# Kernel tuning notes

Measured on AMD Instinct MI355X. Metric: run time of the kernel, lower is better.

## Reference

```python
import jax, jax.numpy as jnp
import numpy as np

NG = 8       # GroupNorm groups
EPS = 1e-5   # torch default eps for GroupNorm/BatchNorm
M_AND = 5    # Anderson history size
MAX_ITER = 25
LAM = 1e-4
BETA = 1.0


def conv2d(x, w):
    # x: [B,C,H,W], w: [O,I,3,3], stride 1, SAME padding (pad=1)
    return jax.lax.conv_general_dilated(x, w, (1, 1), 'SAME',
                                        dimension_numbers=('NCHW', 'OIHW', 'NCHW'))


def group_norm(x, g, b):
    B, C, H, W = x.shape
    xg = x.reshape(B, NG, C // NG, H, W)
    mu = xg.mean((2, 3, 4), keepdims=True)
    var = xg.var((2, 3, 4), keepdims=True)
    xn = ((xg - mu) * jax.lax.rsqrt(var + EPS)).reshape(B, C, H, W)
    return xn * g[None, :, None, None] + b[None, :, None, None]


def batch_norm(x, g, b):
    # training-mode BatchNorm2d: batch statistics over (B,H,W)
    mu = x.mean((0, 2, 3), keepdims=True)
    var = x.var((0, 2, 3), keepdims=True)
    return (x - mu) * jax.lax.rsqrt(var + EPS) * g[None, :, None, None] + b[None, :, None, None]


def resnet_f(p, z, x):
    # y = norm1(relu(conv1(z))); out = norm3(relu(z + norm2(x + conv2(y))))
    y = group_norm(jax.nn.relu(conv2d(z, p['conv1_w'])), p['gn1_g'], p['gn1_b'])
    return group_norm(jax.nn.relu(z + group_norm(x + conv2d(y, p['conv2_w']),
                                                 p['gn2_g'], p['gn2_b'])),
                      p['gn3_g'], p['gn3_b'])


def anderson(f, x0, m=M_AND, lam=LAM, max_iter=MAX_ITER, beta=BETA):
    # Anderson acceleration for fixed point z = f(z); fixed iteration count
    # (the torch version early-exits at tol=0.01; we run the full max_iter for
    # a deterministic jit-friendly reference).
    shape = x0.shape
    bsz = shape[0]
    flat = lambda v: v.reshape(bsz, -1)
    X = [None] * m
    Fv = [None] * m
    X[0] = flat(x0)
    Fv[0] = flat(f(x0))
    X[1] = Fv[0]
    Fv[1] = flat(f(Fv[0].reshape(shape)))
    for k in range(2, max_iter):
        n = min(k, m)
        Xn = jnp.stack(X[:n], 1)   # [B,n,D]
        Fn = jnp.stack(Fv[:n], 1)  # [B,n,D]
        G = Fn - Xn
        Hm = jnp.einsum('bnd,bmd->bnm', G, G) + lam * jnp.eye(n, dtype=x0.dtype)
        Hb = (jnp.zeros((bsz, n + 1, n + 1), x0.dtype)
              .at[:, 1:, 1:].set(Hm)
              .at[:, 0, 1:].set(1.0)
              .at[:, 1:, 0].set(1.0))
        y = jnp.zeros((bsz, n + 1), x0.dtype).at[:, 0].set(1.0)
        alpha = jnp.linalg.solve(Hb, y[..., None])[:, 1:, 0]  # [B,n]
        xk = beta * jnp.einsum('bn,bnd->bd', alpha, Fn) + (1.0 - beta) * jnp.einsum('bn,bnd->bd', alpha, Xn)
        X[k % m] = xk
        Fv[k % m] = flat(f(xk.reshape(shape)))
    return X[(max_iter - 1) % m].reshape(shape)


def setup_inputs() -> dict:
    key = jax.random.key(0)
    ks = jax.random.split(key, 6)
    B, H, W = 8, 128, 200
    f32 = jnp.float32
    return {
        'x': jax.random.normal(ks[0], (B, 1, H, W), f32),
        'conv0_w': jax.random.normal(ks[1], (48, 1, 3, 3), f32) * 0.1,
        'conv0_b': jnp.zeros((48,), f32),
        'bn_g': jnp.ones((48,), f32),
        'bn_b': jnp.zeros((48,), f32),
        'conv1_w': jax.random.normal(ks[2], (64, 48, 3, 3), f32) * 0.01,
        'conv2_w': jax.random.normal(ks[3], (48, 64, 3, 3), f32) * 0.01,
        'gn1_g': jnp.ones((64,), f32), 'gn1_b': jnp.zeros((64,), f32),
        'gn2_g': jnp.ones((48,), f32), 'gn2_b': jnp.zeros((48,), f32),
        'gn3_g': jnp.ones((48,), f32), 'gn3_b': jnp.zeros((48,), f32),
        'fc_w': jax.random.normal(ks[4], (10, 200), f32) * 0.05,
        'fc_b': jnp.zeros((10,), f32),
    }


def reference(x, conv0_w, conv0_b, bn_g, bn_b, conv1_w, conv2_w,
              gn1_g, gn1_b, gn2_g, gn2_b, gn3_g, gn3_b, fc_w, fc_b):
    fp = {'conv1_w': conv1_w, 'conv2_w': conv2_w,
          'gn1_g': gn1_g, 'gn1_b': gn1_b,
          'gn2_g': gn2_g, 'gn2_b': gn2_b,
          'gn3_g': gn3_g, 'gn3_b': gn3_b}
    h = batch_norm(conv2d(x, conv0_w) + conv0_b[None, :, None, None], bn_g, bn_b)
    z_star = anderson(lambda z: resnet_f(fp, z, h), jnp.zeros_like(h))
    z = resnet_f(fp, z_star, h)  # one extra application, as in DEQFixedPoint
    # Linear(200,10) acts on last dim: [B,48,H,200] -> [B,48,H,10]
    return jnp.einsum('bchw,ow->bcho', z, fc_w) + fc_b
```

## Files before the change

### kernel.cpp

```cpp
#include <hip/hip_runtime.h>

#define BB   8
#define HH   128
#define WW   200
#define HWSZ 25600
#define C48  48
#define C64  64
#define NGRP 8
#define EPSV 1e-5f
#define LAMV 1e-4
#define SLOT 9830400
#define DPB  1228800
#define Y64SZ 13107200
#define BIGELEMS 131072000ull

typedef unsigned short bf16_t;
typedef __attribute__((ext_vector_type(4))) short s4v;
typedef __attribute__((ext_vector_type(8))) short s8v;
typedef __attribute__((ext_vector_type(16))) float f32x16;

__device__ inline float b2f(bf16_t b) { return __uint_as_float(((unsigned)b) << 16); }
__device__ inline bf16_t f2b(float f) {
    unsigned u = __float_as_uint(f);
    unsigned r = u + 0x7fffu + ((u >> 16) & 1u);
    return (bf16_t)(r >> 16);
}
__device__ inline float lo16(unsigned u) { return __uint_as_float(u << 16); }
__device__ inline float hi16(unsigned u) { return __uint_as_float(u & 0xffff0000u); }
__device__ inline unsigned pack2(float lo, float hi) {
    return ((unsigned)f2b(lo)) | (((unsigned)f2b(hi)) << 16);
}
__device__ inline float4 ld4(const bf16_t* p) {
    ushort4 u = *(const ushort4*)p;
    return make_float4(b2f(u.x), b2f(u.y), b2f(u.z), b2f(u.w));
}
__device__ inline void st4(bf16_t* p, float4 v) {
    ushort4 u; u.x = f2b(v.x); u.y = f2b(v.y); u.z = f2b(v.z); u.w = f2b(v.w);
    *(ushort4*)p = u;
}
__device__ inline void ld8(const bf16_t* p, float* v) {
    uint4 u = *(const uint4*)p;
    v[0] = lo16(u.x); v[1] = hi16(u.x); v[2] = lo16(u.y); v[3] = hi16(u.y);
    v[4] = lo16(u.z); v[5] = hi16(u.z); v[6] = lo16(u.w); v[7] = hi16(u.w);
}
__device__ inline void st8(bf16_t* p, const float* v) {
    uint4 u;
    u.x = pack2(v[0], v[1]); u.y = pack2(v[2], v[3]);
    u.z = pack2(v[4], v[5]); u.w = pack2(v[6], v[7]);
    *(uint4*)p = u;
}

__device__ inline void ms_from(const double* __restrict__ ds, int pair, double invcnt,
                               float& mean, float& inv) {
    double s = ds[2 * pair], q = ds[2 * pair + 1];
    double m = s * invcnt;
    double v = q * invcnt - m * m;
    mean = (float)m;
    inv = (float)(1.0 / sqrt(v + (double)EPSV));
}


__global__ void zero_kernel(float* __restrict__ p, int n) {
    int i = blockIdx.x * 256 + threadIdx.x;
    if (i < n) p[i] = 0.f;
}
__global__ void fill16_kernel(float4* __restrict__ p) {
    float4 z; z.x = z.y = z.z = z.w = 0.f;
    p[(size_t)blockIdx.x * 256 + threadIdx.x] = z;
}
__global__ void copy16_kernel(float4* __restrict__ dst, const float4* __restrict__ src) {
    size_t i = (size_t)blockIdx.x * 256 + threadIdx.x;
    dst[i] = src[i];
}

__global__ void pack_kernel(const float* __restrict__ w, bf16_t* __restrict__ apk,
                            int CIN, int CO_real, int total) {
    int idx = blockIdx.x * 256 + threadIdx.x;
    if (idx >= total) return;
    int j   = idx & 7;
    int l   = (idx >> 3) & 63;
    int mt  = (idx >> 9) & 1;
    int tap = (idx >> 10) % 9;
    int kc  = idx / 9216;
    int co = mt * 32 + (l & 31);
    int ci = kc * 16 + (l >> 5) * 8 + j;
    float v = (co < CO_real) ? w[((size_t)co * CIN + ci) * 9 + tap] : 0.f;
    apk[idx] = f2b(v);
}

__global__ __launch_bounds__(256) void conv0_kernel(
    const float* __restrict__ x, const float* __restrict__ w0,
    const float* __restrict__ b0, float* __restrict__ out)
{
    __shared__ float xs[3 * 202];
    __shared__ float wt[480];
    const int tid = threadIdx.x;
    const int bI = blockIdx.x / HH, y = blockIdx.x % HH;
    for (int i = tid; i < 606; i += 256) {
        int r = i / 202, cc = i % 202;
        int gy = y + r - 1, gx = cc - 1;
        float v = 0.f;
        if ((unsigned)gy < (unsigned)HH && (unsigned)gx < (unsigned)WW)
            v = x[(size_t)bI * HWSZ + gy * WW + gx];
        xs[r * 202 + cc] = v;
    }
    for (int i = tid; i < 480; i += 256) wt[i] = (i < 432) ? w0[i] : b0[i - 432];
    __syncthreads();
    const size_t obase = (((size_t)bI * HH + y) * WW) * 48;
    for (int ch = tid; ch < 2400; ch += 256) {
        int px = (ch * 4) / 48, c0 = (ch * 4) % 48;
        float xv[3][3];
        #pragma unroll
        for (int r = 0; r < 3; r++)
            #pragma unroll
            for (int dx = 0; dx < 3; dx++)
                xv[r][dx] = xs[r * 202 + px + dx];
        float4 o;
        #pragma unroll
        for (int j = 0; j < 4; j++) {
            int c = c0 + j;
            float acc = wt[432 + c];
            #pragma unroll
            for (int r = 0; r < 3; r++)
                #pragma unroll
                for (int dx = 0; dx < 3; dx++)
                    acc = fmaf(xv[r][dx], wt[c * 9 + r * 3 + dx], acc);
            ((float*)&o)[j] = acc;
        }
        *(float4*)(out + obase + ch * 4) = o;
    }
}

__global__ void bn_stats_kernel(const float* __restrict__ src, double* __restrict__ dst)
{
    __shared__ float ss[192], qq[192];
    const int tid = threadIdx.x;
    const int c = tid % 48, r = tid / 48;
    const int b = blockIdx.y;
    const size_t base = ((size_t)b * HWSZ + (size_t)blockIdx.x * 256) * 48 + c;
    float s = 0.f, q = 0.f;
    for (int p = r; p < 256; p += 4) {
        float v = src[base + (size_t)p * 48];
        s += v; q += v * v;
    }
    ss[tid] = s; qq[tid] = q;
    __syncthreads();
    if (tid < 48) {
        s = ss[tid] + ss[tid + 48] + ss[tid + 96] + ss[tid + 144];
        q = qq[tid] + qq[tid + 48] + qq[tid + 96] + qq[tid + 144];
        unsafeAtomicAdd(&dst[tid * 2],     (double)s);
        unsafeAtomicAdd(&dst[tid * 2 + 1], (double)q);
    }
}

__global__ __launch_bounds__(256) void bn_apply_kernel(
    const float* __restrict__ src, bf16_t* __restrict__ dst,
    const float* __restrict__ gamma, const float* __restrict__ beta,
    const double* __restrict__ ds)
{
    __shared__ float gaT[48], beT[48];
    int tid = threadIdx.x;
    if (tid < 48) {
        float mean, inv; ms_from(ds, tid, 1.0 / 204800.0, mean, inv);
        float ga = gamma[tid] * inv;
        gaT[tid] = ga; beT[tid] = beta[tid] - mean * ga;
    }
    __syncthreads();
    size_t base = (size_t)blockIdx.x * 1024 + (size_t)tid * 4;
    int c0 = (int)(base % 48);
    float4 v = *(const float4*)(src + base);
    ushort4 o;
    o.x = f2b(fmaf(v.x, gaT[c0],     beT[c0]));
    o.y = f2b(fmaf(v.y, gaT[c0 + 1], beT[c0 + 1]));
    o.z = f2b(fmaf(v.z, gaT[c0 + 2], beT[c0 + 2]));
    o.w = f2b(fmaf(v.w, gaT[c0 + 3], beT[c0 + 3]));
    *(ushort4*)(dst + base) = o;
}

template<int CIN, int CIPAD, int CO, int OTS, int CG, bool RELU, bool ADDH, bool FOLDGN>
__global__ __launch_bounds__(512) void conv_mfma_kernel(
    const bf16_t* __restrict__ in, const s8v* __restrict__ apk,
    const bf16_t* __restrict__ hadd, bf16_t* __restrict__ out,
    double* __restrict__ dsOut,
    const double* __restrict__ dsPrev, const float* __restrict__ gPrev,
    const float* __restrict__ bPrev)
{
    constexpr int KC  = CIN / 16;
    constexpr int NC8 = CIN / 8;
    const int tid  = threadIdx.x;
    const int lane = tid & 63;
    const int wv   = tid >> 6;
    const int x0 = blockIdx.x * 32;
    const int y0 = blockIdx.y * 8;
    const int b  = blockIdx.z;

    __shared__ __align__(16) bf16_t bt[10 * 34 * CIPAD];
    __shared__ __align__(16) float gaT[FOLDGN ? CIN : 4];
    __shared__ __align__(16) float beT[FOLDGN ? CIN : 4];
    __shared__ float ss[512], qq[512];

    if (FOLDGN) {
        if (tid < CIN) {
            float mean, inv;
            ms_from(dsPrev, b * NGRP + tid / (CIN / NGRP), 1.0 / 204800.0, mean, inv);
            float ga = gPrev[tid] * inv;
            gaT[tid] = ga; beT[tid] = bPrev[tid] - mean * ga;
        }
        __syncthreads();
    }
    for (int i = tid; i < 10 * 34 * NC8; i += 512) {
        int ch8 = i % NC8, p = i / NC8;
        int r = p / 34, c = p - r * 34;
        int gy = y0 + r - 1, gx = x0 + c - 1;
        s8v v;
        #pragma unroll
        for (int e = 0; e < 8; e++) v[e] = 0;
        if ((unsigned)gy < (unsigned)HH && (unsigned)gx < (unsigned)WW) {
            v = *(const s8v*)(in + ((((size_t)b * HH + gy) * WW + gx) * CIN + ch8 * 8));
            if (FOLDGN) {
                const float* ga8 = &gaT[ch8 * 8];
                const float* be8 = &beT[ch8 * 8];
                float f[8];
                #pragma unroll
                for (int e = 0; e < 8; e++)
                    f[e] = fmaf(b2f((bf16_t)(unsigned short)v[e]), ga8[e], be8[e]);
                unsigned p01, p23, p45, p67;
                asm("v_cvt_pk_bf16_f32 %0, %1, %2" : "=v"(p01) : "v"(f[0]), "v"(f[1]));
                asm("v_cvt_pk_bf16_f32 %0, %1, %2" : "=v"(p23) : "v"(f[2]), "v"(f[3]));
                asm("v_cvt_pk_bf16_f32 %0, %1, %2" : "=v"(p45) : "v"(f[4]), "v"(f[5]));
                asm("v_cvt_pk_bf16_f32 %0, %1, %2" : "=v"(p67) : "v"(f[6]), "v"(f[7]));
                unsigned* vp = (unsigned*)&v;
                vp[0] = p01; vp[1] = p23; vp[2] = p45; vp[3] = p67;
            }
        }
        *(s8v*)(bt + p * CIPAD + ch8 * 8) = v;
    }
    __syncthreads();

    const int n = lane & 31, half = lane >> 5;
    f32x16 acc0, acc1;
    #pragma unroll
    for (int i = 0; i < 16; i++) { acc0[i] = 0.f; acc1[i] = 0.f; }

    #pragma unroll
    for (int ky = 0; ky < 3; ky++)
    #pragma unroll
    for (int kx = 0; kx < 3; kx++) {
        const int tap = ky * 3 + kx;
        s8v af[2 * KC];
        #pragma unroll
        for (int kc = 0; kc < KC; kc++) {
            af[2 * kc]     = apk[(size_t)kc * 1152 + tap * 128 + lane];
            af[2 * kc + 1] = apk[(size_t)kc * 1152 + tap * 128 + 64 + lane];
        }
        const bf16_t* brow = bt + ((wv + ky) * 34 + n + kx) * CIPAD + half * 8;
        #pragma unroll
        for (int kc = 0; kc < KC; kc++) {
            s8v bfrag = *(const s8v*)(brow + kc * 16);
            acc0 = __builtin_amdgcn_mfma_f32_32x32x16_bf16(af[2 * kc],     bfrag, acc0, 0, 0, 0);
            acc1 = __builtin_amdgcn_mfma_f32_32x32x16_bf16(af[2 * kc + 1], bfrag, acc1, 0, 0, 0);
        }
    }
    __syncthreads();

    bf16_t* ot = bt;
    {
        const int pxl = wv * 32 + n;
        const bool pv = (x0 + n) < WW;
        #pragma unroll
        for (int g4 = 0; g4 < 4; g4++) {
            s4v pk0;
            #pragma unroll
            for (int jj = 0; jj < 4; jj++) {
                float v = acc0[g4 * 4 + jj];
                if (RELU) v = fmaxf(v, 0.f);
                pk0[jj] = (short)(pv ? f2b(v) : (bf16_t)0);
            }
            *(s4v*)&ot[pxl * OTS + g4 * 8 + 4 * half] = pk0;
            const int c1b = 32 + g4 * 8 + 4 * half;
            if (c1b + 3 < CO) {
                s4v pk1;
                #pragma unroll
                for (int jj = 0; jj < 4; jj++) {
                    float v = acc1[g4 * 4 + jj];
                    if (RELU) v = fmaxf(v, 0.f);
                    pk1[jj] = (short)(pv ? f2b(v) : (bf16_t)0);
                }
                *(s4v*)&ot[pxl * OTS + c1b] = pk1;
            }
        }
    }
    __syncthreads();
    {
        constexpr int NCH8 = 256 * CO / 8;
        for (int ch = tid; ch < NCH8; ch += 512) {
            int pxl = ch / (CO / 8);
            int co0 = (ch % (CO / 8)) * 8;
            int row = pxl >> 5, col = pxl & 31;
            int xx = x0 + col;
            if (xx < WW) {
                bf16_t* lp = &ot[pxl * OTS + co0];
                size_t ga = (((size_t)b * HH + y0 + row) * WW + xx) * CO + co0;
                if (ADDH) {
                    float4 h0 = ld4(hadd + ga), h1 = ld4(hadd + ga + 4);
                    float4 l0 = ld4(lp), l1 = ld4(lp + 4);
                    float4 v0 = make_float4(l0.x + h0.x, l0.y + h0.y, l0.z + h0.z, l0.w + h0.w);
                    float4 v1 = make_float4(l1.x + h1.x, l1.y + h1.y, l1.z + h1.z, l1.w + h1.w);
                    st4(out + ga, v0); st4(out + ga + 4, v1);
                    st4(lp, v0); st4(lp + 4, v1);
                } else {
                    *(ushort4*)(out + ga)     = *(ushort4*)lp;
                    *(ushort4*)(out + ga + 4) = *(ushort4*)(lp + 4);
                }
            }
        }
    }
    if (ADDH) __syncthreads();
    {
        constexpr int NPH = 512 / CO;
        const int c = tid % CO, rr = tid / CO;
        float s = 0.f, q = 0.f;
        if (rr < NPH) {
            for (int px = rr; px < 256; px += NPH) {
                float v = b2f(ot[px * OTS + c]);
                s += v; q += v * v;
            }
        }
        ss[tid] = s; qq[tid] = q;
        __syncthreads();
        if (tid < CO) {
            float S = ss[tid], Q = qq[tid];
            #pragma unroll
            for (int p = 1; p < NPH; p++) { S += ss[tid + p * CO]; Q += qq[tid + p * CO]; }
            ss[tid] = S; qq[tid] = Q;
        }
        __syncthreads();
        if (tid < NGRP) {
            float S = 0.f, Q = 0.f;
            #pragma unroll
            for (int j = 0; j < CG; j++) { S += ss[tid * CG + j]; Q += qq[tid * CG + j]; }
            unsafeAtomicAdd(&dsOut[((size_t)b * NGRP + tid) * 2],     (double)S);
            unsafeAtomicAdd(&dsOut[((size_t)b * NGRP + tid) * 2 + 1], (double)Q);
        }
    }
}

__global__ __launch_bounds__(192) void add_relu_gn2_kernel(
    bf16_t* __restrict__ u, const bf16_t* __restrict__ z,
    const double* __restrict__ ds2, const float* __restrict__ g2,
    const float* __restrict__ b2, double* __restrict__ ds3)
{
    __shared__ float sm[16];
    const int tid = threadIdx.x;
    const int c0 = 8 * (tid % 6), pxr = tid / 6;
    const int b = blockIdx.y;
    if (tid < 16) sm[tid] = 0.f;
    const int gA = c0 / 6;
    const int split = (gA + 1) * 6 - c0;
    float meanA, invA, meanB, invB;
    ms_from(ds2, b * NGRP + gA,     1.0 / 153600.0, meanA, invA);
    ms_from(ds2, b * NGRP + gA + 1, 1.0 / 153600.0, meanB, invB);
    float wga[8], wbe[8];
    #pragma unroll
    for (int e = 0; e < 8; e++) {
        int c = c0 + e;
        float m = (e < split) ? meanA : meanB, iv = (e < split) ? invA : invB;
        float ga = g2[c] * iv;
        wga[e] = ga; wbe[e] = b2[c] - m * ga;
    }
    __syncthreads();
    const size_t pxbase = (size_t)b * HWSZ + (size_t)blockIdx.x * 256;
    float sA = 0.f, qA = 0.f, sB = 0.f, qB = 0.f;
    for (int it = 0; it < 8; it++) {
        size_t idx = (pxbase + it * 32 + pxr) * 48 + c0;
        float uu[8], zz[8], vv[8];
        ld8(u + idx, uu); ld8(z + idx, zz);
        #pragma unroll
        for (int e = 0; e < 8; e++) {
            float v = fmaxf(fmaf(uu[e], wga[e], wbe[e]) + zz[e], 0.f);
            vv[e] = v;
            if (e < split) { sA += v; qA += v * v; } else { sB += v; qB += v * v; }
        }
        st8(u + idx, vv);
    }
    atomicAdd(&sm[2 * gA], sA);     atomicAdd(&sm[2 * gA + 1], qA);
    atomicAdd(&sm[2 * gA + 2], sB); atomicAdd(&sm[2 * gA + 3], qB);
    __syncthreads();
    if (tid < NGRP) {
        unsafeAtomicAdd(&ds3[(b * NGRP + tid) * 2],     (double)sm[tid * 2]);
        unsafeAtomicAdd(&ds3[(b * NGRP + tid) * 2 + 1], (double)sm[tid * 2 + 1]);
    }
}

__global__ __launch_bounds__(192) void gn3_gram_kernel(
    const bf16_t* __restrict__ v, const bf16_t* __restrict__ z,
    bf16_t* __restrict__ F, bf16_t* __restrict__ G,
    const double* __restrict__ ds3, const float* __restrict__ g3,
    const float* __restrict__ b3,
    const bf16_t* __restrict__ Gall, int jslot, int nf, double* __restrict__ gram)
{
    __shared__ double red[3][5];
    const int tid = threadIdx.x;
    const int c0 = 8 * (tid % 6), pxr = tid / 6;
    const int b = blockIdx.y;
    const int gA = c0 / 6;
    const int split = (gA + 1) * 6 - c0;
    float meanA, invA, meanB, invB;
    ms_from(ds3, b * NGRP + gA,     1.0 / 153600.0, meanA, invA);
    ms_from(ds3, b * NGRP + gA + 1, 1.0 / 153600.0, meanB, invB);
    float wga[8], wbe[8];
    #pragma unroll
    for (int e = 0; e < 8; e++) {
        int c = c0 + e;
        float m = (e < split) ? meanA : meanB, iv = (e < split) ? invA : invB;
        float ga = g3[c] * iv;
        wga[e] = ga; wbe[e] = b3[c] - m * ga;
    }
    const size_t pxbase = (size_t)b * HWSZ + (size_t)blockIdx.x * 256;
    double dot[5] = {0.0, 0.0, 0.0, 0.0, 0.0};
    for (int it = 0; it < 8; it++) {
        size_t idx = (pxbase + it * 32 + pxr) * 48 + c0;
        float rr[8];
        ld8(v + idx, rr);
        #pragma unroll
        for (int e = 0; e < 8; e++) rr[e] = fmaf(rr[e], wga[e], wbe[e]);
        st8(F + idx, rr);
        if (nf > 0) {
            float zz[8], gg[8];
            ld8(z + idx, zz);
            #pragma unroll
            for (int e = 0; e < 8; e++) gg[e] = rr[e] - zz[e];
            st8(G + idx, gg);
            #pragma unroll
            for (int i = 0; i < 5; i++) {
                if (i >= nf) continue;
                float d = 0.f;
                if (i == jslot) {
                    #pragma unroll
                    for (int e = 0; e < 8; e++) d = fmaf(gg[e], gg[e], d);
                } else {
                    float gi[8];
                    ld8(Gall + (size_t)i * SLOT + idx, gi);
                    #pragma unroll
                    for (int e = 0; e < 8; e++) d = fmaf(gg[e], gi[e], d);
                }
                dot[i] += (double)d;
            }
        }
    }
    if (nf > 0) {
        #pragma unroll
        for (int i = 0; i < 5; i++) {
            if (i >= nf) continue;
            #pragma unroll
            for (int off = 32; off > 0; off >>= 1) dot[i] += __shfl_down(dot[i], off);
        }
        int wv = tid >> 6;
        if ((tid & 63) == 0) {
            #pragma unroll
            for (int i = 0; i < 5; i++) if (i < nf) red[wv][i] = dot[i];
        }
        __syncthreads();
        if (tid == 0) {
            #pragma unroll
            for (int i = 0; i < 5; i++) {
                if (i >= nf) continue;
                double D = red[0][i] + red[1][i] + red[2][i];
                unsafeAtomicAdd(&gram[b * 25 + jslot * 5 + i], D);
                if (i != jslot) unsafeAtomicAdd(&gram[b * 25 + i * 5 + jslot], D);
            }
        }
    }
}

__global__ void solve_kernel(const double* __restrict__ gram, float* __restrict__ alpha, int n) {
    int b = threadIdx.x;
    if (b >= BB) return;
    const int m = n + 1;
    double A[6][7];
    for (int i = 0; i < m; i++)
        for (int jj = 0; jj <= m; jj++) A[i][jj] = 0.0;
    for (int i = 1; i < m; i++) { A[0][i] = 1.0; A[i][0] = 1.0; }
    for (int i = 1; i < m; i++)
        for (int jj = 1; jj < m; jj++)
            A[i][jj] = gram[b * 25 + (i - 1) * 5 + (jj - 1)] + ((i == jj) ? LAMV : 0.0);
    A[0][m] = 1.0;
    for (int col = 0; col < m; col++) {
        int piv = col; double best = fabs(A[col][col]);
        for (int rr = col + 1; rr < m; rr++) {
            double tv = fabs(A[rr][col]);
            if (tv > best) { best = tv; piv = rr; }
        }
        if (piv != col)
            for (int cc = col; cc <= m; cc++) {
                double tmp = A[col][cc]; A[col][cc] = A[piv][cc]; A[piv][cc] = tmp;
            }
        double invp = 1.0 / A[col][col];
        for (int cc = col; cc <= m; cc++) A[col][cc] *= invp;
        for (int rr = 0; rr < m; rr++) {
            if (rr == col) continue;
            double f = A[rr][col];
            if (f != 0.0)
                for (int cc = col; cc <= m; cc++) A[rr][cc] = fma(-f, A[col][cc], A[rr][cc]);
        }
    }
    for (int i = 0; i < n; i++) alpha[b * 5 + i] = (float)A[i + 1][m];
}

__global__ __launch_bounds__(256) void xk_kernel(
    const bf16_t* __restrict__ Fb, const float* __restrict__ alpha,
    bf16_t* __restrict__ zcur, int n, double* __restrict__ gram, int jz, int nf)
{
    if (blockIdx.x == 0 && threadIdx.x < 8 * nf) {
        int b = threadIdx.x / nf, i = threadIdx.x % nf;
        gram[b * 25 + jz * 5 + i] = 0.0;
        gram[b * 25 + i * 5 + jz] = 0.0;
    }
    const int b = blockIdx.x / 300;
    float al[5];
    #pragma unroll
    for (int j = 0; j < 5; j++) al[j] = (j < n) ? alpha[b * 5 + j] : 0.f;
    const size_t base = (size_t)blockIdx.x * 4096 + (size_t)threadIdx.x * 8;
    for (int it = 0; it < 2; it++) {
        size_t idx = base + (size_t)it * 2048;
        float s[8] = {0.f, 0.f, 0.f, 0.f, 0.f, 0.f, 0.f, 0.f};
        #pragma unroll
        for (int j = 0; j < 5; j++) {
            if (j < n) {
                float f[8];
                ld8(Fb + (size_t)j * SLOT + idx, f);
                #pragma unroll
                for (int e = 0; e < 8; e++) s[e] = fmaf(f[e], al[j], s[e]);
            }
        }
        st8(zcur + idx, s);
    }
}

__global__ __launch_bounds__(512) void fc_kernel(
    const bf16_t* __restrict__ zf, const float* __restrict__ fw,
    const float* __restrict__ fb, float* __restrict__ out)
{
    __shared__ bf16_t row[9600];
    __shared__ float fwT[2000];
    int tid = threadIdx.x;
    int b = blockIdx.x >> 7, hh = blockIdx.x & 127;
    size_t base = (((size_t)b * HH + hh) * WW) * 48;
    for (int i = tid; i < 2400; i += 512)
        *(ushort4*)&row[i * 4] = *(const ushort4*)(zf + base + (size_t)i * 4);
    for (int i = tid; i < 2000; i += 512) fwT[i] = fw[i];
    __syncthreads();
    if (tid < 480) {
        int c = tid % 48, o = tid / 48;
        float acc = fb[o];
        #pragma unroll 4
        for (int w = 0; w < 200; w++)
            acc = fmaf(b2f(row[w * 48 + c]), fwT[o * 200 + w], acc);
        out[(((size_t)b * 48 + c) * HH + hh) * 10 + o] = acc;
    }
}


static inline int imin(int a, int b) { return a < b ? a : b; }

extern "C" void kernel_launch(void* const* d_in, const int* in_sizes, int n_in,
                              void* d_out, int out_size, void* d_ws, size_t ws_size,
                              hipStream_t stream)
{
    const float* x   = (const float*)d_in[0];
    const float* w0  = (const float*)d_in[1];
    const float* b0  = (const float*)d_in[2];
    const float* bng = (const float*)d_in[3];
    const float* bnb = (const float*)d_in[4];
    const float* w1  = (const float*)d_in[5];
    const float* w2  = (const float*)d_in[6];
    const float* g1  = (const float*)d_in[7];
    const float* be1 = (const float*)d_in[8];
    const float* g2  = (const float*)d_in[9];
    const float* be2 = (const float*)d_in[10];
    const float* g3  = (const float*)d_in[11];
    const float* be3 = (const float*)d_in[12];
    const float* fcw = (const float*)d_in[13];
    const float* fcb = (const float*)d_in[14];
    float* out = (float*)d_out;

    bf16_t* h    = (bf16_t*)d_ws;
    bf16_t* zcur = h + (size_t)SLOT;
    bf16_t* y64  = zcur + (size_t)SLOT;
    bf16_t* Fb   = y64 + (size_t)Y64SZ;
    bf16_t* Gb   = Fb + 5 * (size_t)SLOT;
    double* dstats = (double*)((char*)d_ws + BIGELEMS * 2);
    double* gram   = dstats + 9696;
    float*  alpha  = (float*)(gram + 200);
    bf16_t* apk1   = (bf16_t*)(alpha + 40);
    bf16_t* apk2   = apk1 + 27648;
    float*  scratch = (float*)Gb;

    const size_t need = BIGELEMS * 2 + 9696 * 8 + 200 * 8 + 40 * 4 + (27648 + 36864) * 2;
    if (ws_size < need) return;

    const dim3 blk(256);
    const int CHUNKS16 = SLOT * 2 / 16 / 256;

    zero_kernel<<<(19792 + 255) / 256, blk, 0, stream>>>((float*)dstats, 19792);
    pack_kernel<<<108, blk, 0, stream>>>(w1, apk1, 48, 64, 27648);
    pack_kernel<<<144, blk, 0, stream>>>(w2, apk2, 64, 48, 36864);
    fill16_kernel<<<CHUNKS16, blk, 0, stream>>>((float4*)zcur);

    conv0_kernel<<<BB * HH, blk, 0, stream>>>(x, w0, b0, scratch);
    bn_stats_kernel<<<dim3(100, BB), dim3(192), 0, stream>>>(scratch, dstats);
    bn_apply_kernel<<<SLOT / 1024, blk, 0, stream>>>(scratch, h, bng, bnb, dstats);

    int call = 0;
    auto resnet = [&](const bf16_t* zin, bf16_t* Fdst, bf16_t* Gdst, int jslot, int nf) {
        double* ds = dstats + 96 + 384 * call;
        call++;
        dim3 cg(7, 16, BB);
        conv_mfma_kernel<48, 56, 64, 66, 8, true, false, false><<<cg, dim3(512), 0, stream>>>(
            zin, (const s8v*)apk1, nullptr, y64, ds, nullptr, nullptr, nullptr);
        conv_mfma_kernel<64, 72, 48, 50, 6, false, true, true><<<cg, dim3(512), 0, stream>>>(
            y64, (const s8v*)apk2, h, Fdst, ds + 128, ds, g1, be1);
        add_relu_gn2_kernel<<<dim3(100, BB), dim3(192), 0, stream>>>(
            Fdst, zin, ds + 128, g2, be2, ds + 256);
        gn3_gram_kernel<<<dim3(100, BB), dim3(192), 0, stream>>>(
            Fdst, zin, Fdst, Gdst, ds + 256, g3, be3, Gb, jslot, nf, gram);
    };

    resnet(zcur, Fb, Gb, 0, 1);
    copy16_kernel<<<CHUNKS16, blk, 0, stream>>>((float4*)zcur, (const float4*)Fb);
    resnet(zcur, Fb + (size_t)SLOT, Gb + (size_t)SLOT, 1, 2);

    for (int k = 2; k <= 24; k++) {
        int n = imin(k, 5);
        int j = k % 5;
        int nf = imin(k + 1, 5);
        solve_kernel<<<1, 64, 0, stream>>>(gram, alpha, n);
        xk_kernel<<<2400, blk, 0, stream>>>(Fb, alpha, zcur, n, gram, j, nf);
        if (k < 24)
            resnet(zcur, Fb + (size_t)j * SLOT, Gb + (size_t)j * SLOT, j, nf);
    }

    resnet(zcur, Fb, nullptr, 0, 0);

    fc_kernel<<<BB * HH, dim3(512), 0, stream>>>(Fb, fcw, fcb, out);
}
```

Measured before the change: 5.066 ms.

## Stage conv weights in LDS per K-chunk and batch halo loads into registers

The conv kernel now copies each 16-channel chunk of packed weights into shared memory once per block, so waves no longer each fetch A-fragments from global memory. The loop is reordered to go over K-chunks first, then taps. The halo tile is loaded first into a register array and then written to LDS, which puts all global loads in flight before any LDS stores. Launch bounds now request 4 blocks per CU. In exchange the change adds an 18 KB LDS buffer and more syncs per chunk, which may limit occupancy.

Measured after the change: 4.683 ms. -7.6%, faster.

```diff
diff --git a/kernel.cpp b/kernel.cpp
--- a/kernel.cpp
+++ b/kernel.cpp
@@ -178,7 +178,7 @@
 }
 
 template<int CIN, int CIPAD, int CO, int OTS, int CG, bool RELU, bool ADDH, bool FOLDGN>
-__global__ __launch_bounds__(512) void conv_mfma_kernel(
+__global__ __launch_bounds__(512, 4) void conv_mfma_kernel(
     const bf16_t* __restrict__ in, const s8v* __restrict__ apk,
     const bf16_t* __restrict__ hadd, bf16_t* __restrict__ out,
     double* __restrict__ dsOut,
@@ -187,6 +187,8 @@
 {
     constexpr int KC  = CIN / 16;
     constexpr int NC8 = CIN / 8;
+    constexpr int NITEMS = 10 * 34 * NC8;
+    constexpr int NIT = (NITEMS + 511) / 512;
     const int tid  = threadIdx.x;
     const int lane = tid & 63;
     const int wv   = tid >> 6;
@@ -195,6 +197,7 @@
     const int b  = blockIdx.z;
 
     __shared__ __align__(16) bf16_t bt[10 * 34 * CIPAD];
+    __shared__ __align__(16) s8v ws[1152];
     __shared__ __align__(16) float gaT[FOLDGN ? CIN : 4];
     __shared__ __align__(16) float beT[FOLDGN ? CIN : 4];
     __shared__ float ss[512], qq[512];
@@ -208,16 +211,33 @@
         }
         __syncthreads();
     }
-    for (int i = tid; i < 10 * 34 * NC8; i += 512) {
+
+    s8v vreg[NIT];
+    #pragma unroll
+    for (int k = 0; k < NIT; k++) {
+        int i = tid + k * 512;
+        s8v t;
+        #pragma unroll
+        for (int e = 0; e < 8; e++) t[e] = 0;
+        if (i < NITEMS) {
+            int ch8 = i % NC8, p = i / NC8;
+            int r = p / 34, c = p - r * 34;
+            int gy = y0 + r - 1, gx = x0 + c - 1;
+            if ((unsigned)gy < (unsigned)HH && (unsigned)gx < (unsigned)WW)
+                t = *(const s8v*)(in + ((((size_t)b * HH + gy) * WW + gx) * CIN + ch8 * 8));
+        }
+        vreg[k] = t;
+    }
+    #pragma unroll
+    for (int k = 0; k < NIT; k++) {
+        int i = tid + k * 512;
+        if (i >= NITEMS) continue;
         int ch8 = i % NC8, p = i / NC8;
-        int r = p / 34, c = p - r * 34;
-        int gy = y0 + r - 1, gx = x0 + c - 1;
-        s8v v;
-        #pragma unroll
-        for (int e = 0; e < 8; e++) v[e] = 0;
-        if ((unsigned)gy < (unsigned)HH && (unsigned)gx < (unsigned)WW) {
-            v = *(const s8v*)(in + ((((size_t)b * HH + gy) * WW + gx) * CIN + ch8 * 8));
-            if (FOLDGN) {
+        s8v v = vreg[k];
+        if (FOLDGN) {
+            int r = p / 34, c = p - r * 34;
+            int gy = y0 + r - 1, gx = x0 + c - 1;
+            if ((unsigned)gy < (unsigned)HH && (unsigned)gx < (unsigned)WW) {
                 const float* ga8 = &gaT[ch8 * 8];
                 const float* be8 = &beT[ch8 * 8];
                 float f[8];
@@ -235,7 +255,6 @@
         }
         *(s8v*)(bt + p * CIPAD + ch8 * 8) = v;
     }
-    __syncthreads();
 
     const int n = lane & 31, half = lane >> 5;
     f32x16 acc0, acc1;
@@ -243,22 +262,22 @@
     for (int i = 0; i < 16; i++) { acc0[i] = 0.f; acc1[i] = 0.f; }
 
     #pragma unroll
-    for (int ky = 0; ky < 3; ky++)
-    #pragma unroll
-    for (int kx = 0; kx < 3; kx++) {
-        const int tap = ky * 3 + kx;
-        s8v af[2 * KC];
-        #pragma unroll
-        for (int kc = 0; kc < KC; kc++) {
-            af[2 * kc]     = apk[(size_t)kc * 1152 + tap * 128 + lane];
-            af[2 * kc + 1] = apk[(size_t)kc * 1152 + tap * 128 + 64 + lane];
-        }
-        const bf16_t* brow = bt + ((wv + ky) * 34 + n + kx) * CIPAD + half * 8;
-        #pragma unroll
-        for (int kc = 0; kc < KC; kc++) {
+    for (int kc = 0; kc < KC; kc++) {
+        if (kc) __syncthreads();
+        for (int i = tid; i < 1152; i += 512)
+            ws[i] = apk[(size_t)kc * 1152 + i];
+        __syncthreads();
+        #pragma unroll
+        for (int ky = 0; ky < 3; ky++)
+        #pragma unroll
+        for (int kx = 0; kx < 3; kx++) {
+            const int tap = ky * 3 + kx;
+            s8v a0 = ws[tap * 128 + lane];
+            s8v a1 = ws[tap * 128 + 64 + lane];
+            const bf16_t* brow = bt + ((wv + ky) * 34 + n + kx) * CIPAD + half * 8;
             s8v bfrag = *(const s8v*)(brow + kc * 16);
-            acc0 = __builtin_amdgcn_mfma_f32_32x32x16_bf16(af[2 * kc],     bfrag, acc0, 0, 0, 0);
-            acc1 = __builtin_amdgcn_mfma_f32_32x32x16_bf16(af[2 * kc + 1], bfrag, acc1, 0, 0, 0);
+            acc0 = __builtin_amdgcn_mfma_f32_32x32x16_bf16(a0, bfrag, acc0, 0, 0, 0);
+            acc1 = __builtin_amdgcn_mfma_f32_32x32x16_bf16(a1, bfrag, acc1, 0, 0, 0);
         }
     }
     __syncthreads();
```
